# Performance work log

Hardware: AMD Instinct MI355X
Metric: run time of the kernel (lower is better)

Reference implementation:

```python
import jax, jax.numpy as jnp
import numpy as np

NUM_CLASSES = 80
SCORE_THRESHOLD = 0.05
MAX_DETECTIONS = 300


def setup_inputs() -> dict:
    key = jax.random.key(0)
    k1, k2, k3 = jax.random.split(key, 3)
    B, Q, C = 256, 1000, NUM_CLASSES
    pred_logits = jax.random.normal(k1, (B, Q, C), dtype=jnp.float32)
    # cxcywh boxes in normalized coords (cx,cy in ~(0,1), w,h small positive)
    pred_boxes = jax.random.uniform(k2, (B, Q, 4), dtype=jnp.float32, minval=0.05, maxval=0.6)
    # (height, width) per image, realistic pixel sizes
    target_sizes = jnp.floor(jax.random.uniform(k3, (B, 2), dtype=jnp.float32, minval=224.0, maxval=1024.0))
    return {"pred_logits": pred_logits, "pred_boxes": pred_boxes, "target_sizes": target_sizes}


def reference(pred_logits, pred_boxes, target_sizes):
    # focal-loss path: per-class sigmoid, then max over classes
    prob = jax.nn.sigmoid(pred_logits)                # [B, Q, C]
    scores = jnp.max(prob, axis=-1)                   # [B, Q]
    labels = jnp.argmax(prob, axis=-1)                # [B, Q]

    # cxcywh -> xyxy
    cx, cy, w, h = jnp.split(pred_boxes, 4, axis=-1)  # each [B, Q, 1]
    boxes = jnp.concatenate(
        [cx - 0.5 * w, cy - 0.5 * h, cx + 0.5 * w, cy + 0.5 * h], axis=-1
    )                                                 # [B, Q, 4]

    img_h = target_sizes[:, 0]
    img_w = target_sizes[:, 1]
    scale_fct = jnp.stack([img_w, img_h, img_w, img_h], axis=1)  # [B, 4]
    boxes = boxes * scale_fct[:, None, :]

    # score threshold via sentinel mask, then fixed-size per-image top-k
    masked_scores = jnp.where(scores > SCORE_THRESHOLD, scores, -1.0)
    top_scores, top_idx = jax.lax.top_k(masked_scores, MAX_DETECTIONS)  # [B, K]
    valid = top_scores > SCORE_THRESHOLD                               # [B, K]

    out_scores = jnp.where(valid, top_scores, 0.0)
    out_labels = jnp.where(valid, jnp.take_along_axis(labels, top_idx, axis=1), -1)
    out_boxes = jnp.where(
        valid[..., None],
        jnp.take_along_axis(boxes, top_idx[..., None], axis=1),
        0.0,
    )
    return out_scores, out_labels, out_boxes
```

## Files before the change

kernel.cpp:

```cpp
#include <hip/hip_runtime.h>
#include <math.h>

#define BATCH   256
#define NQ      1000
#define NC      80
#define NDET    300
#define SCORE_TH 0.05f

#define QB        128
#define A_THREADS 256
#define F4Q       20

__global__ __launch_bounds__(A_THREADS) void rtdetr_phase1(
    const float* __restrict__ logits,
    unsigned long long* __restrict__ keys64)
{
    __shared__ float s_val[QB * F4Q];
    __shared__ int   s_cls[QB * F4Q];

    const int bb = blockIdx.x;
    const int b  = bb >> 3;
    const int cb = bb & 7;
    const int q0 = cb * QB;
    const int nq  = min(QB, NQ - q0);
    const int nf4 = nq * F4Q;

    const float4* g = (const float4*)(logits + (size_t)b * NQ * NC) + (size_t)q0 * F4Q;
    const int t = threadIdx.x;

    #pragma unroll
    for (int k = 0; k < 10; ++k) {
        int j = t + k * A_THREADS;
        if (j < nf4) {
            float4 v = g[j];
            float bv = v.x; int bc = 0;
            if (v.y > bv) { bv = v.y; bc = 1; }
            if (v.z > bv) { bv = v.z; bc = 2; }
            if (v.w > bv) { bv = v.w; bc = 3; }
            s_val[j] = bv;
            s_cls[j] = bc;
        }
    }
    __syncthreads();

    if (t < nq) {
        const float* rv = &s_val[t * F4Q];
        const int*   rc = &s_cls[t * F4Q];
        float bv = rv[0];
        int   bc = rc[0];
        #pragma unroll
        for (int i = 1; i < F4Q; ++i) {
            float v = rv[i];
            if (v > bv) { bv = v; bc = 4 * i + rc[i]; }
        }
        float sc = 1.0f / (1.0f + expf(-bv));
        unsigned int key = (sc > SCORE_TH) ? __float_as_uint(sc) : 0u;
        int q = q0 + t;
        keys64[(size_t)b * NQ + q] =
            ((unsigned long long)key << 32) |
            ((unsigned int)(1023 - q) << 10) | (unsigned int)bc;
    }
}

#define B_THREADS 1024

__global__ __launch_bounds__(B_THREADS) void rtdetr_phase2(
    const unsigned long long* __restrict__ keys64,
    const float* __restrict__ boxes,
    const float* __restrict__ sizes,
    float* __restrict__ out)
{
    __shared__ unsigned long long s_k[B_THREADS];

    const int b = blockIdx.x;
    const int t = threadIdx.x;

    s_k[t] = (t < NQ) ? keys64[(size_t)b * NQ + t] : 0ull;
    __syncthreads();

    for (int k = 2; k <= B_THREADS; k <<= 1) {
        for (int j = k >> 1; j > 0; j >>= 1) {
            int ixj = t ^ j;
            if (ixj > t) {
                unsigned long long a = s_k[t];
                unsigned long long c = s_k[ixj];
                bool desc = ((t & k) == 0);
                if (desc ? (a < c) : (a > c)) { s_k[t] = c; s_k[ixj] = a; }
            }
            __syncthreads();
        }
    }

    if (t < NDET) {
        unsigned long long c = s_k[t];
        unsigned int key = (unsigned int)(c >> 32);

        float* out_scores = out;
        float* out_labels = out + (size_t)BATCH * NDET;
        float* out_boxes  = out + (size_t)2 * BATCH * NDET;
        const int o = b * NDET + t;

        if (key != 0u) {
            int lab = (int)(c & 0x3FFull);
            int idx = 1023 - (int)((c >> 10) & 0x3FFull);
            out_scores[o] = __uint_as_float(key);
            out_labels[o] = (float)lab;
            float4 bx = ((const float4*)boxes)[b * NQ + idx];
            const float img_h = sizes[2 * b + 0];
            const float img_w = sizes[2 * b + 1];
            float4 ob;
            ob.x = (bx.x - 0.5f * bx.z) * img_w;
            ob.y = (bx.y - 0.5f * bx.w) * img_h;
            ob.z = (bx.x + 0.5f * bx.z) * img_w;
            ob.w = (bx.y + 0.5f * bx.w) * img_h;
            ((float4*)out_boxes)[o] = ob;
        } else {
            out_scores[o] = 0.0f;
            out_labels[o] = -1.0f;
            ((float4*)out_boxes)[o] = make_float4(0.0f, 0.0f, 0.0f, 0.0f);
        }
    }
}

extern "C" void kernel_launch(void* const* d_in, const int* in_sizes, int n_in,
                              void* d_out, int out_size, void* d_ws, size_t ws_size,
                              hipStream_t stream) {
    const float* logits = (const float*)d_in[0];
    const float* boxes  = (const float*)d_in[1];
    const float* sizes  = (const float*)d_in[2];
    float* out = (float*)d_out;

    unsigned long long* keys64 = (unsigned long long*)d_ws;

    rtdetr_phase1<<<BATCH * 8, A_THREADS, 0, stream>>>(logits, keys64);
    rtdetr_phase2<<<BATCH, B_THREADS, 0, stream>>>(keys64, boxes, sizes, out);
}
```

Before: 135.3 us.

## Use wavefront shuffles for per-query argmax and in-register bitonic sort steps

```diff
diff --git a/kernel.cpp b/kernel.cpp
--- a/kernel.cpp
+++ b/kernel.cpp
@@ -7,93 +7,83 @@
 #define NDET    300
 #define SCORE_TH 0.05f
 
-#define QB        128
+typedef unsigned long long u64;
+
 #define A_THREADS 256
-#define F4Q       20
 
 __global__ __launch_bounds__(A_THREADS) void rtdetr_phase1(
     const float* __restrict__ logits,
-    unsigned long long* __restrict__ keys64)
+    u64* __restrict__ keys64)
 {
-    __shared__ float s_val[QB * F4Q];
-    __shared__ int   s_cls[QB * F4Q];
+    const int t    = threadIdx.x;
+    const int lane = t & 63;
+    const int wid  = t >> 6;
+    const int b    = blockIdx.x >> 4;
+    const int q    = (blockIdx.x & 15) * 64 + wid * 16 + (lane >> 2);
+    const int r    = lane & 3;
 
-    const int bb = blockIdx.x;
-    const int b  = bb >> 3;
-    const int cb = bb & 7;
-    const int q0 = cb * QB;
-    const int nq  = min(QB, NQ - q0);
-    const int nf4 = nq * F4Q;
+    if (q >= NQ) return;
 
-    const float4* g = (const float4*)(logits + (size_t)b * NQ * NC) + (size_t)q0 * F4Q;
-    const int t = threadIdx.x;
+    const float4* g = (const float4*)(logits + (size_t)b * NQ * NC) + (size_t)q * 20;
 
+    float bv = -1e30f;
+    int   bc = 0;
     #pragma unroll
-    for (int k = 0; k < 10; ++k) {
-        int j = t + k * A_THREADS;
-        if (j < nf4) {
-            float4 v = g[j];
-            float bv = v.x; int bc = 0;
-            if (v.y > bv) { bv = v.y; bc = 1; }
-            if (v.z > bv) { bv = v.z; bc = 2; }
-            if (v.w > bv) { bv = v.w; bc = 3; }
-            s_val[j] = bv;
-            s_cls[j] = bc;
-        }
+    for (int i = 0; i < 5; ++i) {
+        float4 v = g[4 * i + r];
+        int c = 16 * i + 4 * r;
+        if (v.x > bv) { bv = v.x; bc = c + 0; }
+        if (v.y > bv) { bv = v.y; bc = c + 1; }
+        if (v.z > bv) { bv = v.z; bc = c + 2; }
+        if (v.w > bv) { bv = v.w; bc = c + 3; }
     }
-    __syncthreads();
-
-    if (t < nq) {
-        const float* rv = &s_val[t * F4Q];
-        const int*   rc = &s_cls[t * F4Q];
-        float bv = rv[0];
-        int   bc = rc[0];
-        #pragma unroll
-        for (int i = 1; i < F4Q; ++i) {
-            float v = rv[i];
-            if (v > bv) { bv = v; bc = 4 * i + rc[i]; }
-        }
+    #pragma unroll
+    for (int d = 1; d <= 2; d <<= 1) {
+        float ov = __shfl_xor(bv, d);
+        int   oc = __shfl_xor(bc, d);
+        if (ov > bv || (ov == bv && oc < bc)) { bv = ov; bc = oc; }
+    }
+    if (r == 0) {
         float sc = 1.0f / (1.0f + expf(-bv));
         unsigned int key = (sc > SCORE_TH) ? __float_as_uint(sc) : 0u;
-        int q = q0 + t;
         keys64[(size_t)b * NQ + q] =
-            ((unsigned long long)key << 32) |
-            ((unsigned int)(1023 - q) << 10) | (unsigned int)bc;
+            ((u64)key << 32) | ((unsigned int)(1023 - q) << 10) | (unsigned int)bc;
     }
 }
 
 #define B_THREADS 1024
 
 __global__ __launch_bounds__(B_THREADS) void rtdetr_phase2(
-    const unsigned long long* __restrict__ keys64,
+    const u64* __restrict__ keys64,
     const float* __restrict__ boxes,
     const float* __restrict__ sizes,
     float* __restrict__ out)
 {
-    __shared__ unsigned long long s_k[B_THREADS];
+    __shared__ u64 s_k[B_THREADS];
 
     const int b = blockIdx.x;
     const int t = threadIdx.x;
 
-    s_k[t] = (t < NQ) ? keys64[(size_t)b * NQ + t] : 0ull;
-    __syncthreads();
+    u64 v = (t < NQ) ? keys64[(size_t)b * NQ + t] : 0ull;
 
     for (int k = 2; k <= B_THREADS; k <<= 1) {
         for (int j = k >> 1; j > 0; j >>= 1) {
-            int ixj = t ^ j;
-            if (ixj > t) {
-                unsigned long long a = s_k[t];
-                unsigned long long c = s_k[ixj];
-                bool desc = ((t & k) == 0);
-                if (desc ? (a < c) : (a > c)) { s_k[t] = c; s_k[ixj] = a; }
+            u64 o;
+            if (j >= 64) {
+                s_k[t] = v;
+                __syncthreads();
+                o = s_k[t ^ j];
+                __syncthreads();
+            } else {
+                o = __shfl_xor(v, j);
             }
-            __syncthreads();
+            const bool takeMax = (((t & j) == 0) == ((t & k) == 0));
+            if (takeMax ? (o > v) : (o < v)) v = o;
         }
     }
 
     if (t < NDET) {
-        unsigned long long c = s_k[t];
-        unsigned int key = (unsigned int)(c >> 32);
+        unsigned int key = (unsigned int)(v >> 32);
 
         float* out_scores = out;
         float* out_labels = out + (size_t)BATCH * NDET;
@@ -101,8 +91,8 @@
         const int o = b * NDET + t;
 
         if (key != 0u) {
-            int lab = (int)(c & 0x3FFull);
-            int idx = 1023 - (int)((c >> 10) & 0x3FFull);
+            int lab = (int)(v & 0x3FFull);
+            int idx = 1023 - (int)((v >> 10) & 0x3FFull);
             out_scores[o] = __uint_as_float(key);
             out_labels[o] = (float)lab;
             float4 bx = ((const float4*)boxes)[b * NQ + idx];
@@ -130,8 +120,8 @@
     const float* sizes  = (const float*)d_in[2];
     float* out = (float*)d_out;
 
-    unsigned long long* keys64 = (unsigned long long*)d_ws;
+    u64* keys64 = (u64*)d_ws;
 
-    rtdetr_phase1<<<BATCH * 8, A_THREADS, 0, stream>>>(logits, keys64);
+    rtdetr_phase1<<<BATCH * 16, A_THREADS, 0, stream>>>(logits, keys64);
     rtdetr_phase2<<<BATCH, B_THREADS, 0, stream>>>(keys64, boxes, sizes, out);
 }
```

Measured after the change: 133.7 us. About the same (-1.1%).
